# Optimization experiments

Measured on AMD Instinct MI355X. Metric: run time of the kernel, lower is better.

The kernel has to match this reference:

```python
import jax, jax.numpy as jnp
import numpy as np

N = 591   # number of drugs (hardcoded in the original module)
FD = 1024 # args.fd
E = 120000


def setup_inputs() -> dict:
    key = jax.random.key(0)
    ks = jax.random.split(key, 32)
    s = 1.0 / np.sqrt(FD).astype(np.float32)
    inp = {}
    inp['dm1'] = jax.random.normal(ks[0], (N, FD), jnp.float32)
    for i, v in enumerate(['t', 's', 'g']):
        inp['edges_' + v] = jax.random.randint(ks[1 + i], (2, E), 0, N)
        inp['ew_' + v] = jax.random.uniform(ks[4 + i], (E,), jnp.float32)
    for i, nm in enumerate(['t1', 't2', 's1', 's2', 'g1', 'g2']):
        inp['W_' + nm] = jax.random.normal(ks[7 + i], (FD, FD), jnp.float32) * s
        inp['b_' + nm] = jnp.zeros((FD,), jnp.float32)
    inp['fc1_w'] = jax.random.normal(ks[20], (30, 6), jnp.float32) * 0.4
    inp['fc1_b'] = jnp.zeros((30,), jnp.float32)
    inp['fc2_w'] = jax.random.normal(ks[21], (6, 30), jnp.float32) * 0.2
    inp['fc2_b'] = jnp.zeros((6,), jnp.float32)
    inp['conv_w'] = jax.random.normal(ks[22], (6,), jnp.float32) * 0.4
    inp['conv_b'] = jnp.zeros((), jnp.float32)
    return inp


def gcn(x, W, b, src, dst, ew):
    """PyG GCNConv: x@W, add self-loops (weight 1), symmetric norm, scatter-add, +bias."""
    xw = x @ W                                   # [N, FD]
    loop = jnp.arange(N)
    src2 = jnp.concatenate([src, loop])
    dst2 = jnp.concatenate([dst, loop])
    ew2 = jnp.concatenate([ew, jnp.ones((N,), ew.dtype)])
    deg = jax.ops.segment_sum(ew2, dst2, num_segments=N)
    dinv = jnp.where(deg > 0, jax.lax.rsqrt(deg), 0.0)
    norm = dinv[src2] * ew2 * dinv[dst2]         # [E+N]
    agg = jax.ops.segment_sum(norm[:, None] * xw[src2], dst2, num_segments=N)
    return agg + b


def reference(dm1, edges_t, ew_t, edges_s, ew_s, edges_g, ew_g,
              W_t1, b_t1, W_t2, b_t2, W_s1, b_s1, W_s2, b_s2,
              W_g1, b_g1, W_g2, b_g2,
              fc1_w, fc1_b, fc2_w, fc2_b, conv_w, conv_b):
    def two_layers(e, w, W1, b1, W2, b2):
        h1 = jax.nn.relu(gcn(dm1, W1, b1, e[0], e[1], w))
        h2 = jax.nn.relu(gcn(h1, W2, b2, e[0], e[1], w))
        return h1, h2

    t1, t2 = two_layers(edges_t, ew_t, W_t1, b_t1, W_t2, b_t2)
    s1, s2 = two_layers(edges_s, ew_s, W_s1, b_s1, W_s2, b_s2)
    g1, g2 = two_layers(edges_g, ew_g, W_g1, b_g1, W_g2, b_g2)

    # cat(dim=1).t().view(1, 6, FD, N)  ->  [6, FD, N]
    comb = jnp.stack([t1.T, t2.T, s1.T, s2.T, g1.T, g2.T], axis=0)

    # SE-style channel attention over the 6 channels
    pool = comb.mean(axis=(1, 2))                         # [6]
    h = jax.nn.relu(pool @ fc1_w.T + fc1_b)               # [30]
    a = jax.nn.sigmoid(h @ fc2_w.T + fc2_b)               # [6]
    att = jax.nn.relu(a[:, None, None] * comb)            # [6, FD, N]

    # 1x1 conv (6 -> 1 channel), then view(FD, N).t()
    y = jnp.einsum('c,cfn->fn', conv_w, att) + conv_b     # [FD, N]
    return y.T                                            # [N, FD]
```

## Files before the change

### kernel.cpp

```cpp
#include <hip/hip_runtime.h>

#define NDRUG 591
#define FDIM 1024
#define NEDGE 120000
#define MPAD 640
#define ASTRIDE 349281
#define ABSTRIDE (MPAD*MPAD)
#define HSTRIDE (MPAD*FDIM)
#define REAL (NDRUG*FDIM)
#define WSTRIDE (FDIM*FDIM)

typedef __attribute__((ext_vector_type(8))) short bf16x8;
typedef __attribute__((ext_vector_type(4))) float f32x4;
typedef __attribute__((ext_vector_type(4))) unsigned short u16x4;

static __device__ __forceinline__ unsigned short f2bf(float f) {
    unsigned u = __builtin_bit_cast(unsigned, f);
    u += 0x7fffu + ((u >> 16) & 1u);
    return (unsigned short)(u >> 16);
}
static __device__ __forceinline__ float bf2f(unsigned short h) {
    return __builtin_bit_cast(float, ((unsigned)h) << 16);
}

typedef const __attribute__((address_space(1))) unsigned int* gp1_t;
typedef __attribute__((address_space(3))) unsigned int* lp3_t;
static __device__ __forceinline__ void gload16(const void* g, unsigned short* l) {
    __builtin_amdgcn_global_load_lds((gp1_t)g, (lp3_t)l, 16, 0, 0);
}

__global__ void init_kernel(float* AmatF, float* scal) {
    int i = blockIdx.x * blockDim.x + threadIdx.x;
    const int TOT = 3 * ASTRIDE;
    int b = i * 4;
    if (b + 3 < TOT) {
        *(float4*)(AmatF + b) = make_float4(0.f, 0.f, 0.f, 0.f);
    } else if (b < TOT) {
        for (int j = b; j < TOT; ++j) AmatF[j] = 0.f;
    }
    if (i < 16) scal[i] = 0.f;
}

__global__ void scatter_kernel(const int* e_t, const float* w_t,
                               const int* e_s, const float* w_s,
                               const int* e_g, const float* w_g, float* AmatF) {
    int i = blockIdx.x * blockDim.x + threadIdx.x;
    const int PER = NEDGE + NDRUG;
    if (i >= 3 * PER) return;
    int g = i / PER, r = i - g * PER;
    float* Ag = AmatF + (long)g * ASTRIDE;
    if (r < NEDGE) {
        const int*   E_ = (g == 0) ? e_t : (g == 1) ? e_s : e_g;
        const float* W_ = (g == 0) ? w_t : (g == 1) ? w_s : w_g;
        int src = E_[r], dst = E_[NEDGE + r];
        atomicAdd(Ag + (long)dst * NDRUG + src, W_[r]);
    } else {
        int n = r - NEDGE;
        atomicAdd(Ag + (long)n * NDRUG + n, 1.0f);
    }
}

__global__ void rowdeg_kernel(const float* AmatF, float* dinv) {
    int r = blockIdx.x, g = blockIdx.y;
    const float* row = AmatF + (long)g * ASTRIDE + (long)r * NDRUG;
    float s = 0.f;
    for (int c = threadIdx.x; c < NDRUG; c += 64) s += row[c];
#pragma unroll
    for (int off = 32; off > 0; off >>= 1) s += __shfl_down(s, off);
    if (threadIdx.x == 0)
        dinv[g * NDRUG + r] = (s > 0.f) ? rsqrtf(s) : 0.f;
}

__global__ void conv_A(const float* AmatF, const float* dinv, unsigned short* Amatb) {
    int r = blockIdx.x, g = blockIdx.y;
    int t = threadIdx.x;
    if (t >= 160) return;
    int c = t * 4;
    u16x4 o = {0, 0, 0, 0};
    if (r < NDRUG) {
        const float* src = AmatF + (long)g * ASTRIDE + (long)r * NDRUG;
        const float* dv = dinv + g * NDRUG;
        float dr = dv[r];
#pragma unroll
        for (int j = 0; j < 4; j++) {
            int cc = c + j;
            if (cc < NDRUG) o[j] = f2bf(src[cc] * dv[cc] * dr);
        }
    }
    *(u16x4*)(Amatb + (long)g * ABSTRIDE + (long)r * MPAD + c) = o;
}

__global__ void conv_dm1(const float* dm1, unsigned short* dm1b) {
    int r = blockIdx.x;
    int c = threadIdx.x * 4;
    u16x4 o = {0, 0, 0, 0};
    if (r < NDRUG) {
        float4 v = *(const float4*)(dm1 + (long)r * FDIM + c);
        o[0] = f2bf(v.x); o[1] = f2bf(v.y); o[2] = f2bf(v.z); o[3] = f2bf(v.w);
    }
    *(u16x4*)(dm1b + (long)r * FDIM + c) = o;
}

__global__ void conv_w6(const float* w0, const float* w1, const float* w2,
                        const float* w3, const float* w4, const float* w5,
                        unsigned short* WTb) {
    __shared__ float s[32][33];
    int z = blockIdx.z;
    const float* W = (z == 0) ? w0 : (z == 1) ? w1 : (z == 2) ? w2
                   : (z == 3) ? w3 : (z == 4) ? w4 : w5;
    unsigned short* WT = WTb + (long)z * WSTRIDE;
    int n0 = blockIdx.x * 32, k0 = blockIdx.y * 32;
    int tx = threadIdx.x & 31, ty = threadIdx.x >> 5;
#pragma unroll
    for (int p = 0; p < 4; p++)
        s[ty + 8 * p][tx] = W[(long)(k0 + ty + 8 * p) * FDIM + n0 + tx];
    __syncthreads();
#pragma unroll
    for (int p = 0; p < 4; p++)
        WT[(long)(n0 + ty + 8 * p) * FDIM + k0 + tx] = f2bf(s[tx][ty + 8 * p]);
}

template <int EPI>
__global__ __launch_bounds__(256) void mfma_gemm(
    const unsigned short* __restrict__ Abase, long strideA, int ldaK,
    const unsigned short* __restrict__ Bbase, long strideB, int ldbK,
    const float* __restrict__ bias0, const float* __restrict__ bias1,
    const float* __restrict__ bias2,
    unsigned short* __restrict__ Cbase, long strideC, int ldC, int K,
    float* __restrict__ poolacc, int layer)
{
    __shared__ unsigned short ldsA[2][4096];
    __shared__ unsigned short ldsB[2][4096];
    __shared__ float red[4];

    const int g = blockIdx.z;
    const unsigned short* A = Abase + (long)g * strideA;
    const unsigned short* B = Bbase + (long)g * strideB;
    unsigned short* C = Cbase + (long)g * strideC;
    const float* bias = (g == 0) ? bias0 : (g == 1) ? bias1 : bias2;

    const int m0 = blockIdx.y * 64;
    const int n0 = blockIdx.x * 64;
    const int tid = threadIdx.x;
    const int w = tid >> 6, lane = tid & 63;
    const int l15 = lane & 15, lq = lane >> 4;
    const int wm = w >> 1, wn = w & 1;

    const int sr  = lane >> 3;
    const int kcs = 8 * ((lane & 7) ^ sr);
    const int segA0 = 2 * w, segA1 = 2 * w + 1;
    const int rA0 = segA0 * 8 + sr, rA1 = segA1 * 8 + sr;

    int offA[2][2], offB[2][2];
    {
        int ra0 = 32 * wm + l15, ra1 = ra0 + 16;
        int rb0 = 32 * wn + l15, rb1 = rb0 + 16;
        offA[0][0] = ra0 * 64 + ((lq    ) ^ (ra0 & 7)) * 8;
        offA[0][1] = ra0 * 64 + ((lq + 4) ^ (ra0 & 7)) * 8;
        offA[1][0] = ra1 * 64 + ((lq    ) ^ (ra1 & 7)) * 8;
        offA[1][1] = ra1 * 64 + ((lq + 4) ^ (ra1 & 7)) * 8;
        offB[0][0] = rb0 * 64 + ((lq    ) ^ (rb0 & 7)) * 8;
        offB[0][1] = rb0 * 64 + ((lq + 4) ^ (rb0 & 7)) * 8;
        offB[1][0] = rb1 * 64 + ((lq    ) ^ (rb1 & 7)) * 8;
        offB[1][1] = rb1 * 64 + ((lq + 4) ^ (rb1 & 7)) * 8;
    }

    f32x4 acc00 = {0.f, 0.f, 0.f, 0.f}, acc01 = {0.f, 0.f, 0.f, 0.f};
    f32x4 acc10 = {0.f, 0.f, 0.f, 0.f}, acc11 = {0.f, 0.f, 0.f, 0.f};

    const int nt = K >> 6;

#define STAGE(bf, k0c) do {                                                        \
    gload16(A + (long)(m0 + rA0) * ldaK + (k0c) + kcs, &ldsA[bf][segA0 * 512]);    \
    gload16(A + (long)(m0 + rA1) * ldaK + (k0c) + kcs, &ldsA[bf][segA1 * 512]);    \
    gload16(B + (long)(n0 + rA0) * ldbK + (k0c) + kcs, &ldsB[bf][segA0 * 512]);    \
    gload16(B + (long)(n0 + rA1) * ldbK + (k0c) + kcs, &ldsB[bf][segA1 * 512]);    \
} while (0)

    STAGE(0, 0);

    for (int t = 0; t < nt; ++t) {
        const int cur = t & 1;
        if (t + 1 < nt) {
            STAGE(cur ^ 1, (t + 1) << 6);
            asm volatile("s_waitcnt vmcnt(4)");
        } else {
            asm volatile("s_waitcnt vmcnt(0)");
        }
        __builtin_amdgcn_s_barrier();
        __builtin_amdgcn_sched_barrier(0);
        const unsigned short* pa = ldsA[cur];
        const unsigned short* pb = ldsB[cur];
        {
            bf16x8 a0 = *(const bf16x8*)(pa + offA[0][0]);
            bf16x8 a1 = *(const bf16x8*)(pa + offA[1][0]);
            bf16x8 b0 = *(const bf16x8*)(pb + offB[0][0]);
            bf16x8 b1 = *(const bf16x8*)(pb + offB[1][0]);
            acc00 = __builtin_amdgcn_mfma_f32_16x16x32_bf16(a0, b0, acc00, 0, 0, 0);
            acc01 = __builtin_amdgcn_mfma_f32_16x16x32_bf16(a0, b1, acc01, 0, 0, 0);
            acc10 = __builtin_amdgcn_mfma_f32_16x16x32_bf16(a1, b0, acc10, 0, 0, 0);
            acc11 = __builtin_amdgcn_mfma_f32_16x16x32_bf16(a1, b1, acc11, 0, 0, 0);
        }
        {
            bf16x8 a0 = *(const bf16x8*)(pa + offA[0][1]);
            bf16x8 a1 = *(const bf16x8*)(pa + offA[1][1]);
            bf16x8 b0 = *(const bf16x8*)(pb + offB[0][1]);
            bf16x8 b1 = *(const bf16x8*)(pb + offB[1][1]);
            acc00 = __builtin_amdgcn_mfma_f32_16x16x32_bf16(a0, b0, acc00, 0, 0, 0);
            acc01 = __builtin_amdgcn_mfma_f32_16x16x32_bf16(a0, b1, acc01, 0, 0, 0);
            acc10 = __builtin_amdgcn_mfma_f32_16x16x32_bf16(a1, b0, acc10, 0, 0, 0);
            acc11 = __builtin_amdgcn_mfma_f32_16x16x32_bf16(a1, b1, acc11, 0, 0, 0);
        }
        asm volatile("s_waitcnt lgkmcnt(0)");
        __builtin_amdgcn_sched_barrier(0);
        __builtin_amdgcn_s_barrier();
    }
#undef STAGE

    if (EPI == 0) {
#define TSTORE(accv, mo, no) do {                                   \
        int nn = n0 + 32 * wn + (no) * 16 + l15;                    \
        int mm = m0 + 32 * wm + (mo) * 16 + lq * 4;                 \
        u16x4 pk;                                                   \
        pk[0] = f2bf(accv[0]); pk[1] = f2bf(accv[1]);               \
        pk[2] = f2bf(accv[2]); pk[3] = f2bf(accv[3]);               \
        *(u16x4*)&C[(long)nn * ldC + mm] = pk;                      \
} while (0)
        TSTORE(acc00, 0, 0); TSTORE(acc01, 0, 1);
        TSTORE(acc10, 1, 0); TSTORE(acc11, 1, 1);
#undef TSTORE
    } else {
        float spool = 0.f;
#define NSTORE(accv, mo, no) do {                                   \
        int nn = n0 + 32 * wn + (no) * 16 + l15;                    \
        int mm = m0 + 32 * wm + (mo) * 16 + lq * 4;                 \
        float bs = bias[nn];                                        \
        _Pragma("unroll")                                           \
        for (int i = 0; i < 4; i++) {                               \
            float v = fmaxf(accv[i] + bs, 0.f);                     \
            C[(long)(mm + i) * ldC + nn] = f2bf(v);                 \
            if (mm + i < NDRUG) spool += v;                         \
        }                                                           \
} while (0)
        NSTORE(acc00, 0, 0); NSTORE(acc01, 0, 1);
        NSTORE(acc10, 1, 0); NSTORE(acc11, 1, 1);
#undef NSTORE
#pragma unroll
        for (int off = 32; off > 0; off >>= 1) spool += __shfl_down(spool, off);
        if (lane == 0) red[w] = spool;
        __syncthreads();
        if (tid == 0)
            atomicAdd(poolacc + 2 * g + layer, red[0] + red[1] + red[2] + red[3]);
    }
}

__global__ void mlp_kernel(const float* acc, const float* fc1w, const float* fc1b,
                           const float* fc2w, const float* fc2b, const float* convw,
                           float* wout) {
    __shared__ float hsh[30], plsh[6];
    int t = threadIdx.x;
    const float inv = 1.0f / (float)REAL;
    if (t < 6) plsh[t] = acc[t] * inv;
    __syncthreads();
    if (t < 30) {
        float s = fc1b[t];
#pragma unroll
        for (int c = 0; c < 6; c++) s += plsh[c] * fc1w[t * 6 + c];
        hsh[t] = fmaxf(s, 0.f);
    }
    __syncthreads();
    float hv = (t < 30) ? hsh[t] : 0.f;
    for (int j = 0; j < 6; j++) {
        float p = (t < 30) ? hv * fc2w[j * 30 + t] : 0.f;
#pragma unroll
        for (int off = 32; off > 0; off >>= 1) p += __shfl_down(p, off);
        if (t == 0) {
            float s = fc2b[j] + p;
            wout[j] = convw[j] / (1.f + expf(-s));
        }
    }
}

__global__ void combine_kernel(const unsigned short* h1b, const unsigned short* h2b,
                               const float* wv, const float* convb, float* out) {
    int i = blockIdx.x * 256 + threadIdx.x;
    const int nv = REAL / 8;
    if (i >= nv) return;
    float cb = convb[0];
    float r[8];
#pragma unroll
    for (int j = 0; j < 8; j++) r[j] = cb;
#define ACCCH(c, ptr) do {                                          \
        float wc = wv[c];                                           \
        bf16x8 v = *(const bf16x8*)((ptr) + (long)i * 8);           \
        _Pragma("unroll")                                           \
        for (int j = 0; j < 8; j++) r[j] += wc * bf2f((unsigned short)v[j]); \
} while (0)
    ACCCH(0, h1b);
    ACCCH(1, h2b);
    ACCCH(2, h1b + HSTRIDE);
    ACCCH(3, h2b + HSTRIDE);
    ACCCH(4, h1b + 2 * HSTRIDE);
    ACCCH(5, h2b + 2 * HSTRIDE);
#undef ACCCH
    float4 o0 = make_float4(r[0], r[1], r[2], r[3]);
    float4 o1 = make_float4(r[4], r[5], r[6], r[7]);
    *(float4*)(out + (long)i * 8) = o0;
    *(float4*)(out + (long)i * 8 + 4) = o1;
}

extern "C" void kernel_launch(void* const* d_in, const int* in_sizes, int n_in,
                              void* d_out, int out_size, void* d_ws, size_t ws_size,
                              hipStream_t stream) {
    const float* dm1 = (const float*)d_in[0];
    const int*   e_t = (const int*)d_in[1];
    const float* w_t = (const float*)d_in[2];
    const int*   e_s = (const int*)d_in[3];
    const float* w_s = (const float*)d_in[4];
    const int*   e_g = (const int*)d_in[5];
    const float* w_g = (const float*)d_in[6];
    const float* W_t1 = (const float*)d_in[7];
    const float* b_t1 = (const float*)d_in[8];
    const float* W_t2 = (const float*)d_in[9];
    const float* b_t2 = (const float*)d_in[10];
    const float* W_s1 = (const float*)d_in[11];
    const float* b_s1 = (const float*)d_in[12];
    const float* W_s2 = (const float*)d_in[13];
    const float* b_s2 = (const float*)d_in[14];
    const float* W_g1 = (const float*)d_in[15];
    const float* b_g1 = (const float*)d_in[16];
    const float* W_g2 = (const float*)d_in[17];
    const float* b_g2 = (const float*)d_in[18];
    const float* fc1w = (const float*)d_in[19];
    const float* fc1b = (const float*)d_in[20];
    const float* fc2w = (const float*)d_in[21];
    const float* fc2b = (const float*)d_in[22];
    const float* convw = (const float*)d_in[23];
    const float* convb = (const float*)d_in[24];
    float* out = (float*)d_out;

    char* base = (char*)d_ws;
    unsigned short* WTb = (unsigned short*)base;
    float* AmatF = (float*)base;
    unsigned short* h2b = (unsigned short*)(base + (size_t)3 * WSTRIDE * 2);
    size_t o = (size_t)6 * WSTRIDE * 2;
    float* dinv = (float*)(base + o); o += 8192;
    float* scal = (float*)(base + o); o += 256;
    unsigned short* dm1b  = (unsigned short*)(base + o); o += (size_t)MPAD * FDIM * 2;
    unsigned short* Amatb = (unsigned short*)(base + o); o += (size_t)3 * ABSTRIDE * 2;
    unsigned short* xwT   = (unsigned short*)(base + o); o += (size_t)3 * HSTRIDE * 2;
    unsigned short* h1b   = (unsigned short*)(base + o); o += (size_t)3 * HSTRIDE * 2;
    if (ws_size < o) return;

    init_kernel<<<(3 * ASTRIDE / 4 + 256) / 256, 256, 0, stream>>>(AmatF, scal);
    scatter_kernel<<<(3 * (NEDGE + NDRUG) + 255) / 256, 256, 0, stream>>>(
        e_t, w_t, e_s, w_s, e_g, w_g, AmatF);
    rowdeg_kernel<<<dim3(NDRUG, 3), 64, 0, stream>>>(AmatF, dinv);
    conv_A<<<dim3(MPAD, 3), 256, 0, stream>>>(AmatF, dinv, Amatb);
    conv_w6<<<dim3(32, 32, 6), 256, 0, stream>>>(
        W_t1, W_s1, W_g1, W_t2, W_s2, W_g2, WTb);
    conv_dm1<<<MPAD, 256, 0, stream>>>(dm1, dm1b);

    dim3 gg(FDIM / 64, MPAD / 64, 3);
    mfma_gemm<0><<<gg, 256, 0, stream>>>(
        dm1b, 0L, FDIM, WTb, (long)WSTRIDE, FDIM,
        nullptr, nullptr, nullptr, xwT, (long)HSTRIDE, MPAD, FDIM, scal, 0);
    mfma_gemm<1><<<gg, 256, 0, stream>>>(
        Amatb, (long)ABSTRIDE, MPAD, xwT, (long)HSTRIDE, MPAD,
        b_t1, b_s1, b_g1, h1b, (long)HSTRIDE, FDIM, MPAD, scal, 0);
    mfma_gemm<0><<<gg, 256, 0, stream>>>(
        h1b, (long)HSTRIDE, FDIM, WTb + (size_t)3 * WSTRIDE, (long)WSTRIDE, FDIM,
        nullptr, nullptr, nullptr, xwT, (long)HSTRIDE, MPAD, FDIM, scal, 0);
    mfma_gemm<1><<<gg, 256, 0, stream>>>(
        Amatb, (long)ABSTRIDE, MPAD, xwT, (long)HSTRIDE, MPAD,
        b_t2, b_s2, b_g2, h2b, (long)HSTRIDE, FDIM, MPAD, scal, 1);

    mlp_kernel<<<1, 64, 0, stream>>>(scal, fc1w, fc1b, fc2w, fc2b, convw, scal + 8);
    combine_kernel<<<(REAL / 8 + 255) / 256, 256, 0, stream>>>(h1b, h2b, scal + 8, convb, out);
}
```

Measured before the change: 219.0 us.

## Fuse all stages into one cooperative persistent kernel with grid syncs

Replaces the chain of about twelve kernel launches with a single cooperative kernel of 256 persistent blocks. The blocks step through the stages (zeroing, edge scatter, degree, bf16 conversions, the four GEMM phases, the MLP and the combine) separated by grid.sync, and the original launches remain as a fallback if the cooperative launch fails. This is meant to remove per-launch overhead and the idle gaps between launches. In exchange, parallelism is capped at 256 blocks; the GEMM phases have 480 tiles, so some blocks process two tiles. Each grid barrier also costs time, and the fused kernel may need more registers.

```diff
diff --git a/kernel.cpp b/kernel.cpp
--- a/kernel.cpp
+++ b/kernel.cpp
@@ -1,4 +1,6 @@
 #include <hip/hip_runtime.h>
+#include <hip/hip_cooperative_groups.h>
+namespace cg = cooperative_groups;
 
 #define NDRUG 591
 #define FDIM 1024
@@ -9,6 +11,10 @@
 #define HSTRIDE (MPAD*FDIM)
 #define REAL (NDRUG*FDIM)
 #define WSTRIDE (FDIM*FDIM)
+#define NBLK 256
+#define NTHR 256
+#define GSTR (NBLK*NTHR)
+#define NTILE 480
 
 typedef __attribute__((ext_vector_type(8))) short bf16x8;
 typedef __attribute__((ext_vector_type(4))) float f32x4;
@@ -29,118 +35,15 @@
     __builtin_amdgcn_global_load_lds((gp1_t)g, (lp3_t)l, 16, 0, 0);
 }
 
-__global__ void init_kernel(float* AmatF, float* scal) {
-    int i = blockIdx.x * blockDim.x + threadIdx.x;
-    const int TOT = 3 * ASTRIDE;
-    int b = i * 4;
-    if (b + 3 < TOT) {
-        *(float4*)(AmatF + b) = make_float4(0.f, 0.f, 0.f, 0.f);
-    } else if (b < TOT) {
-        for (int j = b; j < TOT; ++j) AmatF[j] = 0.f;
-    }
-    if (i < 16) scal[i] = 0.f;
-}
-
-__global__ void scatter_kernel(const int* e_t, const float* w_t,
-                               const int* e_s, const float* w_s,
-                               const int* e_g, const float* w_g, float* AmatF) {
-    int i = blockIdx.x * blockDim.x + threadIdx.x;
-    const int PER = NEDGE + NDRUG;
-    if (i >= 3 * PER) return;
-    int g = i / PER, r = i - g * PER;
-    float* Ag = AmatF + (long)g * ASTRIDE;
-    if (r < NEDGE) {
-        const int*   E_ = (g == 0) ? e_t : (g == 1) ? e_s : e_g;
-        const float* W_ = (g == 0) ? w_t : (g == 1) ? w_s : w_g;
-        int src = E_[r], dst = E_[NEDGE + r];
-        atomicAdd(Ag + (long)dst * NDRUG + src, W_[r]);
-    } else {
-        int n = r - NEDGE;
-        atomicAdd(Ag + (long)n * NDRUG + n, 1.0f);
-    }
-}
-
-__global__ void rowdeg_kernel(const float* AmatF, float* dinv) {
-    int r = blockIdx.x, g = blockIdx.y;
-    const float* row = AmatF + (long)g * ASTRIDE + (long)r * NDRUG;
-    float s = 0.f;
-    for (int c = threadIdx.x; c < NDRUG; c += 64) s += row[c];
-#pragma unroll
-    for (int off = 32; off > 0; off >>= 1) s += __shfl_down(s, off);
-    if (threadIdx.x == 0)
-        dinv[g * NDRUG + r] = (s > 0.f) ? rsqrtf(s) : 0.f;
-}
-
-__global__ void conv_A(const float* AmatF, const float* dinv, unsigned short* Amatb) {
-    int r = blockIdx.x, g = blockIdx.y;
-    int t = threadIdx.x;
-    if (t >= 160) return;
-    int c = t * 4;
-    u16x4 o = {0, 0, 0, 0};
-    if (r < NDRUG) {
-        const float* src = AmatF + (long)g * ASTRIDE + (long)r * NDRUG;
-        const float* dv = dinv + g * NDRUG;
-        float dr = dv[r];
-#pragma unroll
-        for (int j = 0; j < 4; j++) {
-            int cc = c + j;
-            if (cc < NDRUG) o[j] = f2bf(src[cc] * dv[cc] * dr);
-        }
-    }
-    *(u16x4*)(Amatb + (long)g * ABSTRIDE + (long)r * MPAD + c) = o;
-}
-
-__global__ void conv_dm1(const float* dm1, unsigned short* dm1b) {
-    int r = blockIdx.x;
-    int c = threadIdx.x * 4;
-    u16x4 o = {0, 0, 0, 0};
-    if (r < NDRUG) {
-        float4 v = *(const float4*)(dm1 + (long)r * FDIM + c);
-        o[0] = f2bf(v.x); o[1] = f2bf(v.y); o[2] = f2bf(v.z); o[3] = f2bf(v.w);
-    }
-    *(u16x4*)(dm1b + (long)r * FDIM + c) = o;
-}
-
-__global__ void conv_w6(const float* w0, const float* w1, const float* w2,
-                        const float* w3, const float* w4, const float* w5,
-                        unsigned short* WTb) {
-    __shared__ float s[32][33];
-    int z = blockIdx.z;
-    const float* W = (z == 0) ? w0 : (z == 1) ? w1 : (z == 2) ? w2
-                   : (z == 3) ? w3 : (z == 4) ? w4 : w5;
-    unsigned short* WT = WTb + (long)z * WSTRIDE;
-    int n0 = blockIdx.x * 32, k0 = blockIdx.y * 32;
-    int tx = threadIdx.x & 31, ty = threadIdx.x >> 5;
-#pragma unroll
-    for (int p = 0; p < 4; p++)
-        s[ty + 8 * p][tx] = W[(long)(k0 + ty + 8 * p) * FDIM + n0 + tx];
-    __syncthreads();
-#pragma unroll
-    for (int p = 0; p < 4; p++)
-        WT[(long)(n0 + ty + 8 * p) * FDIM + k0 + tx] = f2bf(s[tx][ty + 8 * p]);
-}
-
 template <int EPI>
-__global__ __launch_bounds__(256) void mfma_gemm(
-    const unsigned short* __restrict__ Abase, long strideA, int ldaK,
-    const unsigned short* __restrict__ Bbase, long strideB, int ldbK,
-    const float* __restrict__ bias0, const float* __restrict__ bias1,
-    const float* __restrict__ bias2,
-    unsigned short* __restrict__ Cbase, long strideC, int ldC, int K,
-    float* __restrict__ poolacc, int layer)
+static __device__ __forceinline__ void gemm_tile(
+    const unsigned short* __restrict__ A, int ldaK,
+    const unsigned short* __restrict__ B, int ldbK,
+    const float* __restrict__ bias,
+    unsigned short* __restrict__ C, int ldC, int K,
+    float* __restrict__ poolslot, int m0, int n0,
+    unsigned short (&ldsA)[2][4096], unsigned short (&ldsB)[2][4096], float* aux)
 {
-    __shared__ unsigned short ldsA[2][4096];
-    __shared__ unsigned short ldsB[2][4096];
-    __shared__ float red[4];
-
-    const int g = blockIdx.z;
-    const unsigned short* A = Abase + (long)g * strideA;
-    const unsigned short* B = Bbase + (long)g * strideB;
-    unsigned short* C = Cbase + (long)g * strideC;
-    const float* bias = (g == 0) ? bias0 : (g == 1) ? bias1 : bias2;
-
-    const int m0 = blockIdx.y * 64;
-    const int n0 = blockIdx.x * 64;
     const int tid = threadIdx.x;
     const int w = tid >> 6, lane = tid & 63;
     const int l15 = lane & 15, lq = lane >> 4;
@@ -165,9 +68,8 @@
         offB[1][1] = rb1 * 64 + ((lq + 4) ^ (rb1 & 7)) * 8;
     }
 
-    f32x4 acc00 = {0.f, 0.f, 0.f, 0.f}, acc01 = {0.f, 0.f, 0.f, 0.f};
-    f32x4 acc10 = {0.f, 0.f, 0.f, 0.f}, acc11 = {0.f, 0.f, 0.f, 0.f};
-
+    f32x4 acc00 = {0.f,0.f,0.f,0.f}, acc01 = {0.f,0.f,0.f,0.f};
+    f32x4 acc10 = {0.f,0.f,0.f,0.f}, acc11 = {0.f,0.f,0.f,0.f};
     const int nt = K >> 6;
 
 #define STAGE(bf, k0c) do {                                                        \
@@ -178,7 +80,6 @@
 } while (0)
 
     STAGE(0, 0);
-
     for (int t = 0; t < nt; ++t) {
         const int cur = t & 1;
         if (t + 1 < nt) {
@@ -247,11 +148,304 @@
 #undef NSTORE
 #pragma unroll
         for (int off = 32; off > 0; off >>= 1) spool += __shfl_down(spool, off);
-        if (lane == 0) red[w] = spool;
+        if (lane == 0) aux[w] = spool;
         __syncthreads();
-        if (tid == 0)
-            atomicAdd(poolacc + 2 * g + layer, red[0] + red[1] + red[2] + red[3]);
-    }
+        if (tid == 0) atomicAdd(poolslot, aux[0] + aux[1] + aux[2] + aux[3]);
+        __syncthreads();
+    }
+}
+
+struct MegaParams {
+    const float* dm1;
+    const int* et; const float* wt;
+    const int* es; const float* ws;
+    const int* eg; const float* wg;
+    const float* W[6];
+    const float* b1[3]; const float* b2[3];
+    const float* fc1w; const float* fc1b;
+    const float* fc2w; const float* fc2b;
+    const float* convw; const float* convb;
+    float* out;
+    float* AmatF; float* dinv; float* scal;
+    unsigned short* WTb; unsigned short* dm1b; unsigned short* Amatb;
+    unsigned short* xwT; unsigned short* h1b; unsigned short* h2b;
+};
+
+__global__ __launch_bounds__(256, 2) void mega(MegaParams p) {
+    __shared__ unsigned short ldsA[2][4096];
+    __shared__ unsigned short ldsB[2][4096];
+    __shared__ float aux[64];
+    cg::grid_group grid = cg::this_grid();
+    const int b = blockIdx.x, tid = threadIdx.x;
+
+    {
+        const int TOT = 3 * ASTRIDE;
+        for (int i = b * NTHR + tid; i * 4 < TOT; i += GSTR) {
+            int e = i * 4;
+            if (e + 3 < TOT) *(float4*)(p.AmatF + e) = make_float4(0.f, 0.f, 0.f, 0.f);
+            else { for (int j = e; j < TOT; ++j) p.AmatF[j] = 0.f; }
+        }
+        if (b == 0 && tid < 16) p.scal[tid] = 0.f;
+    }
+    grid.sync();
+
+    {
+        const int PER = NEDGE + NDRUG;
+        for (int i = b * NTHR + tid; i < 3 * PER; i += GSTR) {
+            int g = i / PER, r = i - g * PER;
+            float* Ag = p.AmatF + (long)g * ASTRIDE;
+            if (r < NEDGE) {
+                const int*   E_ = (g == 0) ? p.et : (g == 1) ? p.es : p.eg;
+                const float* W_ = (g == 0) ? p.wt : (g == 1) ? p.ws : p.wg;
+                atomicAdd(Ag + (long)E_[NEDGE + r] * NDRUG + E_[r], W_[r]);
+            } else {
+                int n = r - NEDGE;
+                atomicAdd(Ag + (long)n * NDRUG + n, 1.0f);
+            }
+        }
+    }
+    grid.sync();
+
+    {
+        int wv = tid >> 6, lane = tid & 63;
+        for (int row = b * 4 + wv; row < 3 * NDRUG; row += NBLK * 4) {
+            int g = row / NDRUG, r = row - g * NDRUG;
+            const float* src = p.AmatF + (long)g * ASTRIDE + (long)r * NDRUG;
+            float s = 0.f;
+            for (int c = lane; c < NDRUG; c += 64) s += src[c];
+#pragma unroll
+            for (int off = 32; off > 0; off >>= 1) s += __shfl_down(s, off);
+            if (lane == 0) p.dinv[row] = (s > 0.f) ? rsqrtf(s) : 0.f;
+        }
+    }
+    grid.sync();
+
+    {
+        for (int r = b; r < MPAD; r += NBLK) {
+            int c = tid * 4;
+            u16x4 o = {0, 0, 0, 0};
+            if (r < NDRUG) {
+                float4 v = *(const float4*)(p.dm1 + (long)r * FDIM + c);
+                o[0] = f2bf(v.x); o[1] = f2bf(v.y); o[2] = f2bf(v.z); o[3] = f2bf(v.w);
+            }
+            *(u16x4*)(p.dm1b + (long)r * FDIM + c) = o;
+        }
+        for (int it = b; it < 3 * MPAD; it += NBLK) {
+            int g = it / MPAD, r = it - g * MPAD;
+            if (tid < 160) {
+                int c = tid * 4;
+                u16x4 o = {0, 0, 0, 0};
+                if (r < NDRUG) {
+                    const float* src = p.AmatF + (long)g * ASTRIDE + (long)r * NDRUG;
+                    const float* dv = p.dinv + g * NDRUG;
+                    float dr = dv[r];
+#pragma unroll
+                    for (int j = 0; j < 4; j++) {
+                        int cc = c + j;
+                        if (cc < NDRUG) o[j] = f2bf(src[cc] * dv[cc] * dr);
+                    }
+                }
+                *(u16x4*)(p.Amatb + (long)g * ABSTRIDE + (long)r * MPAD + c) = o;
+            }
+        }
+        float* ts = (float*)ldsA;
+        int tx = tid & 31, ty = tid >> 5;
+        for (int tix = b; tix < 6 * 1024; tix += NBLK) {
+            int z = tix >> 10, rem = tix & 1023;
+            int n0w = (rem & 31) * 32, k0w = (rem >> 5) * 32;
+            const float* Wsrc = p.W[z];
+            unsigned short* WT = p.WTb + (long)z * WSTRIDE;
+            __syncthreads();
+#pragma unroll
+            for (int q = 0; q < 4; q++)
+                ts[(ty + 8 * q) * 33 + tx] = Wsrc[(long)(k0w + ty + 8 * q) * FDIM + n0w + tx];
+            __syncthreads();
+#pragma unroll
+            for (int q = 0; q < 4; q++)
+                WT[(long)(n0w + ty + 8 * q) * FDIM + k0w + tx] = f2bf(ts[tx * 33 + ty + 8 * q]);
+        }
+        __syncthreads();
+    }
+    grid.sync();
+
+#define TILE_LOOP(body) for (int tl = b; tl < NTILE; tl += NBLK) { \
+        int g = tl / 160, rr = tl - g * 160;                        \
+        int n0 = (rr & 15) * 64, m0 = (rr >> 4) * 64;               \
+        body;                                                       \
+    }
+
+    TILE_LOOP(gemm_tile<0>(p.dm1b, FDIM, p.WTb + (long)g * WSTRIDE, FDIM, nullptr,
+                           p.xwT + (long)g * HSTRIDE, MPAD, FDIM, nullptr, m0, n0, ldsA, ldsB, aux))
+    grid.sync();
+    TILE_LOOP(gemm_tile<1>(p.Amatb + (long)g * ABSTRIDE, MPAD, p.xwT + (long)g * HSTRIDE, MPAD,
+                           p.b1[g], p.h1b + (long)g * HSTRIDE, FDIM, MPAD,
+                           p.scal + 2 * g, m0, n0, ldsA, ldsB, aux))
+    grid.sync();
+    TILE_LOOP(gemm_tile<0>(p.h1b + (long)g * HSTRIDE, FDIM, p.WTb + (long)(3 + g) * WSTRIDE, FDIM,
+                           nullptr, p.xwT + (long)g * HSTRIDE, MPAD, FDIM, nullptr, m0, n0, ldsA, ldsB, aux))
+    grid.sync();
+    TILE_LOOP(gemm_tile<1>(p.Amatb + (long)g * ABSTRIDE, MPAD, p.xwT + (long)g * HSTRIDE, MPAD,
+                           p.b2[g], p.h2b + (long)g * HSTRIDE, FDIM, MPAD,
+                           p.scal + 2 * g + 1, m0, n0, ldsA, ldsB, aux))
+#undef TILE_LOOP
+    grid.sync();
+
+    if (b == 0) {
+        int t = tid;
+        const float inv = 1.0f / (float)REAL;
+        if (t < 6) aux[32 + t] = p.scal[t] * inv;
+        __syncthreads();
+        if (t < 30) {
+            float s = p.fc1b[t];
+#pragma unroll
+            for (int c = 0; c < 6; c++) s += aux[32 + c] * p.fc1w[t * 6 + c];
+            aux[t] = fmaxf(s, 0.f);
+        }
+        __syncthreads();
+        if (t < 64) {
+            float hv = (t < 30) ? aux[t] : 0.f;
+            for (int j = 0; j < 6; j++) {
+                float pr = (t < 30) ? hv * p.fc2w[j * 30 + t] : 0.f;
+#pragma unroll
+                for (int off = 32; off > 0; off >>= 1) pr += __shfl_down(pr, off);
+                if (t == 0)
+                    p.scal[8 + j] = p.convw[j] / (1.f + expf(-(p.fc2b[j] + pr)));
+            }
+        }
+    }
+    grid.sync();
+
+    {
+        const int nv = REAL / 8;
+        float cb = p.convb[0];
+        float w0 = p.scal[8], w1 = p.scal[9], w2 = p.scal[10];
+        float w3 = p.scal[11], w4 = p.scal[12], w5 = p.scal[13];
+        for (int i = b * NTHR + tid; i < nv; i += GSTR) {
+            float r8[8];
+#pragma unroll
+            for (int j = 0; j < 8; j++) r8[j] = cb;
+#define ACCCH(wc, ptr) do {                                                 \
+            bf16x8 v = *(const bf16x8*)((ptr) + (long)i * 8);               \
+            _Pragma("unroll")                                               \
+            for (int j = 0; j < 8; j++) r8[j] += (wc) * bf2f((unsigned short)v[j]); \
+} while (0)
+            ACCCH(w0, p.h1b);
+            ACCCH(w1, p.h2b);
+            ACCCH(w2, p.h1b + HSTRIDE);
+            ACCCH(w3, p.h2b + HSTRIDE);
+            ACCCH(w4, p.h1b + 2 * HSTRIDE);
+            ACCCH(w5, p.h2b + 2 * HSTRIDE);
+#undef ACCCH
+            *(float4*)(p.out + (long)i * 8)     = make_float4(r8[0], r8[1], r8[2], r8[3]);
+            *(float4*)(p.out + (long)i * 8 + 4) = make_float4(r8[4], r8[5], r8[6], r8[7]);
+        }
+    }
+}
+
+__global__ void init_kernel(float* AmatF, float* scal) {
+    int i = blockIdx.x * blockDim.x + threadIdx.x;
+    const int TOT = 3 * ASTRIDE;
+    int b = i * 4;
+    if (b + 3 < TOT) *(float4*)(AmatF + b) = make_float4(0.f, 0.f, 0.f, 0.f);
+    else if (b < TOT) { for (int j = b; j < TOT; ++j) AmatF[j] = 0.f; }
+    if (i < 16) scal[i] = 0.f;
+}
+
+__global__ void scatter_kernel(const int* e_t, const float* w_t,
+                               const int* e_s, const float* w_s,
+                               const int* e_g, const float* w_g, float* AmatF) {
+    int i = blockIdx.x * blockDim.x + threadIdx.x;
+    const int PER = NEDGE + NDRUG;
+    if (i >= 3 * PER) return;
+    int g = i / PER, r = i - g * PER;
+    float* Ag = AmatF + (long)g * ASTRIDE;
+    if (r < NEDGE) {
+        const int*   E_ = (g == 0) ? e_t : (g == 1) ? e_s : e_g;
+        const float* W_ = (g == 0) ? w_t : (g == 1) ? w_s : w_g;
+        atomicAdd(Ag + (long)E_[NEDGE + r] * NDRUG + E_[r], W_[r]);
+    } else {
+        int n = r - NEDGE;
+        atomicAdd(Ag + (long)n * NDRUG + n, 1.0f);
+    }
+}
+
+__global__ void rowdeg_kernel(const float* AmatF, float* dinv) {
+    int r = blockIdx.x, g = blockIdx.y;
+    const float* row = AmatF + (long)g * ASTRIDE + (long)r * NDRUG;
+    float s = 0.f;
+    for (int c = threadIdx.x; c < NDRUG; c += 64) s += row[c];
+#pragma unroll
+    for (int off = 32; off > 0; off >>= 1) s += __shfl_down(s, off);
+    if (threadIdx.x == 0) dinv[g * NDRUG + r] = (s > 0.f) ? rsqrtf(s) : 0.f;
+}
+
+__global__ void conv_A(const float* AmatF, const float* dinv, unsigned short* Amatb) {
+    int r = blockIdx.x, g = blockIdx.y;
+    int t = threadIdx.x;
+    if (t >= 160) return;
+    int c = t * 4;
+    u16x4 o = {0, 0, 0, 0};
+    if (r < NDRUG) {
+        const float* src = AmatF + (long)g * ASTRIDE + (long)r * NDRUG;
+        const float* dv = dinv + g * NDRUG;
+        float dr = dv[r];
+#pragma unroll
+        for (int j = 0; j < 4; j++) {
+            int cc = c + j;
+            if (cc < NDRUG) o[j] = f2bf(src[cc] * dv[cc] * dr);
+        }
+    }
+    *(u16x4*)(Amatb + (long)g * ABSTRIDE + (long)r * MPAD + c) = o;
+}
+
+__global__ void conv_dm1(const float* dm1, unsigned short* dm1b) {
+    int r = blockIdx.x;
+    int c = threadIdx.x * 4;
+    u16x4 o = {0, 0, 0, 0};
+    if (r < NDRUG) {
+        float4 v = *(const float4*)(dm1 + (long)r * FDIM + c);
+        o[0] = f2bf(v.x); o[1] = f2bf(v.y); o[2] = f2bf(v.z); o[3] = f2bf(v.w);
+    }
+    *(u16x4*)(dm1b + (long)r * FDIM + c) = o;
+}
+
+__global__ void conv_w6(const float* w0, const float* w1, const float* w2,
+                        const float* w3, const float* w4, const float* w5,
+                        unsigned short* WTb) {
+    __shared__ float s[32][33];
+    int z = blockIdx.z;
+    const float* W = (z == 0) ? w0 : (z == 1) ? w1 : (z == 2) ? w2
+                   : (z == 3) ? w3 : (z == 4) ? w4 : w5;
+    unsigned short* WT = WTb + (long)z * WSTRIDE;
+    int n0 = blockIdx.x * 32, k0 = blockIdx.y * 32;
+    int tx = threadIdx.x & 31, ty = threadIdx.x >> 5;
+#pragma unroll
+    for (int q = 0; q < 4; q++)
+        s[ty + 8 * q][tx] = W[(long)(k0 + ty + 8 * q) * FDIM + n0 + tx];
+    __syncthreads();
+#pragma unroll
+    for (int q = 0; q < 4; q++)
+        WT[(long)(n0 + ty + 8 * q) * FDIM + k0 + tx] = f2bf(s[tx][ty + 8 * q]);
+}
+
+template <int EPI>
+__global__ __launch_bounds__(256) void gemm_wrap(
+    const unsigned short* __restrict__ Abase, long strideA, int ldaK,
+    const unsigned short* __restrict__ Bbase, long strideB, int ldbK,
+    const float* __restrict__ bias0, const float* __restrict__ bias1,
+    const float* __restrict__ bias2,
+    unsigned short* __restrict__ Cbase, long strideC, int ldC, int K,
+    float* __restrict__ poolacc, int layer)
+{
+    __shared__ unsigned short ldsA[2][4096];
+    __shared__ unsigned short ldsB[2][4096];
+    __shared__ float aux[64];
+    int g = blockIdx.z;
+    const float* bias = (g == 0) ? bias0 : (g == 1) ? bias1 : bias2;
+    gemm_tile<EPI>(Abase + (long)g * strideA, ldaK, Bbase + (long)g * strideB, ldbK, bias,
+                   Cbase + (long)g * strideC, ldC, K,
+                   poolacc ? poolacc + 2 * g + layer : nullptr,
+                   blockIdx.y * 64, blockIdx.x * 64, ldsA, ldsB, aux);
 }
 
 __global__ void mlp_kernel(const float* acc, const float* fc1w, const float* fc1b,
@@ -271,13 +465,10 @@
     __syncthreads();
     float hv = (t < 30) ? hsh[t] : 0.f;
     for (int j = 0; j < 6; j++) {
-        float p = (t < 30) ? hv * fc2w[j * 30 + t] : 0.f;
-#pragma unroll
-        for (int off = 32; off > 0; off >>= 1) p += __shfl_down(p, off);
-        if (t == 0) {
-            float s = fc2b[j] + p;
-            wout[j] = convw[j] / (1.f + expf(-s));
-        }
+        float pr = (t < 30) ? hv * fc2w[j * 30 + t] : 0.f;
+#pragma unroll
+        for (int off = 32; off > 0; off >>= 1) pr += __shfl_down(pr, off);
+        if (t == 0) wout[j] = convw[j] / (1.f + expf(-(fc2b[j] + pr)));
     }
 }
 
@@ -287,14 +478,14 @@
     const int nv = REAL / 8;
     if (i >= nv) return;
     float cb = convb[0];
-    float r[8];
-#pragma unroll
-    for (int j = 0; j < 8; j++) r[j] = cb;
+    float r8[8];
+#pragma unroll
+    for (int j = 0; j < 8; j++) r8[j] = cb;
 #define ACCCH(c, ptr) do {                                          \
         float wc = wv[c];                                           \
         bf16x8 v = *(const bf16x8*)((ptr) + (long)i * 8);           \
         _Pragma("unroll")                                           \
-        for (int j = 0; j < 8; j++) r[j] += wc * bf2f((unsigned short)v[j]); \
+        for (int j = 0; j < 8; j++) r8[j] += wc * bf2f((unsigned short)v[j]); \
 } while (0)
     ACCCH(0, h1b);
     ACCCH(1, h2b);
@@ -303,78 +494,73 @@
     ACCCH(4, h1b + 2 * HSTRIDE);
     ACCCH(5, h2b + 2 * HSTRIDE);
 #undef ACCCH
-    float4 o0 = make_float4(r[0], r[1], r[2], r[3]);
-    float4 o1 = make_float4(r[4], r[5], r[6], r[7]);
-    *(float4*)(out + (long)i * 8) = o0;
-    *(float4*)(out + (long)i * 8 + 4) = o1;
+    *(float4*)(out + (long)i * 8)     = make_float4(r8[0], r8[1], r8[2], r8[3]);
+    *(float4*)(out + (long)i * 8 + 4) = make_float4(r8[4], r8[5], r8[6], r8[7]);
 }
 
 extern "C" void kernel_launch(void* const* d_in, const int* in_sizes, int n_in,
                               void* d_out, int out_size, void* d_ws, size_t ws_size,
                               hipStream_t stream) {
-    const float* dm1 = (const float*)d_in[0];
-    const int*   e_t = (const int*)d_in[1];
-    const float* w_t = (const float*)d_in[2];
-    const int*   e_s = (const int*)d_in[3];
-    const float* w_s = (const float*)d_in[4];
-    const int*   e_g = (const int*)d_in[5];
-    const float* w_g = (const float*)d_in[6];
-    const float* W_t1 = (const float*)d_in[7];
-    const float* b_t1 = (const float*)d_in[8];
-    const float* W_t2 = (const float*)d_in[9];
-    const float* b_t2 = (const float*)d_in[10];
-    const float* W_s1 = (const float*)d_in[11];
-    const float* b_s1 = (const float*)d_in[12];
-    const float* W_s2 = (const float*)d_in[13];
-    const float* b_s2 = (const float*)d_in[14];
-    const float* W_g1 = (const float*)d_in[15];
-    const float* b_g1 = (const float*)d_in[16];
-    const float* W_g2 = (const float*)d_in[17];
-    const float* b_g2 = (const float*)d_in[18];
-    const float* fc1w = (const float*)d_in[19];
-    const float* fc1b = (const float*)d_in[20];
-    const float* fc2w = (const float*)d_in[21];
-    const float* fc2b = (const float*)d_in[22];
-    const float* convw = (const float*)d_in[23];
-    const float* convb = (const float*)d_in[24];
-    float* out = (float*)d_out;
+    MegaParams p;
+    p.dm1 = (const float*)d_in[0];
+    p.et = (const int*)d_in[1];  p.wt = (const float*)d_in[2];
+    p.es = (const int*)d_in[3];  p.ws = (const float*)d_in[4];
+    p.eg = (const int*)d_in[5];  p.wg = (const float*)d_in[6];
+    p.W[0] = (const float*)d_in[7];   p.b1[0] = (const float*)d_in[8];
+    p.W[3] = (const float*)d_in[9];   p.b2[0] = (const float*)d_in[10];
+    p.W[1] = (const float*)d_in[11];  p.b1[1] = (const float*)d_in[12];
+    p.W[4] = (const float*)d_in[13];  p.b2[1] = (const float*)d_in[14];
+    p.W[2] = (const float*)d_in[15];  p.b1[2] = (const float*)d_in[16];
+    p.W[5] = (const float*)d_in[17];  p.b2[2] = (const float*)d_in[18];
+    p.fc1w = (const float*)d_in[19]; p.fc1b = (const float*)d_in[20];
+    p.fc2w = (const float*)d_in[21]; p.fc2b = (const float*)d_in[22];
+    p.convw = (const float*)d_in[23]; p.convb = (const float*)d_in[24];
+    p.out = (float*)d_out;
 
     char* base = (char*)d_ws;
-    unsigned short* WTb = (unsigned short*)base;
-    float* AmatF = (float*)base;
-    unsigned short* h2b = (unsigned short*)(base + (size_t)3 * WSTRIDE * 2);
-    size_t o = (size_t)6 * WSTRIDE * 2;
-    float* dinv = (float*)(base + o); o += 8192;
-    float* scal = (float*)(base + o); o += 256;
-    unsigned short* dm1b  = (unsigned short*)(base + o); o += (size_t)MPAD * FDIM * 2;
-    unsigned short* Amatb = (unsigned short*)(base + o); o += (size_t)3 * ABSTRIDE * 2;
-    unsigned short* xwT   = (unsigned short*)(base + o); o += (size_t)3 * HSTRIDE * 2;
-    unsigned short* h1b   = (unsigned short*)(base + o); o += (size_t)3 * HSTRIDE * 2;
+    size_t o = 0;
+    auto alloc = [&](size_t bytes) { void* ptr = base + o; o += (bytes + 255) & ~(size_t)255; return ptr; };
+    p.AmatF = (float*)alloc((size_t)3 * ASTRIDE * 4);
+    p.WTb   = (unsigned short*)alloc((size_t)6 * WSTRIDE * 2);
+    p.dinv  = (float*)alloc(8192);
+    p.scal  = (float*)alloc(256);
+    p.dm1b  = (unsigned short*)alloc((size_t)MPAD * FDIM * 2);
+    p.Amatb = (unsigned short*)alloc((size_t)3 * ABSTRIDE * 2);
+    p.xwT   = (unsigned short*)alloc((size_t)3 * HSTRIDE * 2);
+    p.h1b   = (unsigned short*)alloc((size_t)3 * HSTRIDE * 2);
+    p.h2b   = (unsigned short*)alloc((size_t)3 * HSTRIDE * 2);
     if (ws_size < o) return;
 
-    init_kernel<<<(3 * ASTRIDE / 4 + 256) / 256, 256, 0, stream>>>(AmatF, scal);
+    void* args[] = { (void*)&p };
+    hipError_t err = hipLaunchCooperativeKernel((const void*)mega, dim3(NBLK), dim3(NTHR),
+                                                args, 0, stream);
+    if (err == hipSuccess) return;
+
+    init_kernel<<<(3 * ASTRIDE / 4 + 256) / 256, 256, 0, stream>>>(p.AmatF, p.scal);
     scatter_kernel<<<(3 * (NEDGE + NDRUG) + 255) / 256, 256, 0, stream>>>(
-        e_t, w_t, e_s, w_s, e_g, w_g, AmatF);
-    rowdeg_kernel<<<dim3(NDRUG, 3), 64, 0, stream>>>(AmatF, dinv);
-    conv_A<<<dim3(MPAD, 3), 256, 0, stream>>>(AmatF, dinv, Amatb);
+        p.et, p.wt, p.es, p.ws, p.eg, p.wg, p.AmatF);
+    rowdeg_kernel<<<dim3(NDRUG, 3), 64, 0, stream>>>(p.AmatF, p.dinv);
+    conv_A<<<dim3(MPAD, 3), 256, 0, stream>>>(p.AmatF, p.dinv, p.Amatb);
     conv_w6<<<dim3(32, 32, 6), 256, 0, stream>>>(
-        W_t1, W_s1, W_g1, W_t2, W_s2, W_g2, WTb);
-    conv_dm1<<<MPAD, 256, 0, stream>>>(dm1, dm1b);
+        p.W[0], p.W[1], p.W[2], p.W[3], p.W[4], p.W[5], p.WTb);
+    conv_dm1<<<MPAD, 256, 0, stream>>>(p.dm1, p.dm1b);
 
     dim3 gg(FDIM / 64, MPAD / 64, 3);
-    mfma_gemm<0><<<gg, 256, 0, stream>>>(
-        dm1b, 0L, FDIM, WTb, (long)WSTRIDE, FDIM,
-        nullptr, nullptr, nullptr, xwT, (long)HSTRIDE, MPAD, FDIM, scal, 0);
-    mfma_gemm<1><<<gg, 256, 0, stream>>>(
-        Amatb, (long)ABSTRIDE, MPAD, xwT, (long)HSTRIDE, MPAD,
-        b_t1, b_s1, b_g1, h1b, (long)HSTRIDE, FDIM, MPAD, scal, 0);
-    mfma_gemm<0><<<gg, 256, 0, stream>>>(
-        h1b, (long)HSTRIDE, FDIM, WTb + (size_t)3 * WSTRIDE, (long)WSTRIDE, FDIM,
-        nullptr, nullptr, nullptr, xwT, (long)HSTRIDE, MPAD, FDIM, scal, 0);
-    mfma_gemm<1><<<gg, 256, 0, stream>>>(
-        Amatb, (long)ABSTRIDE, MPAD, xwT, (long)HSTRIDE, MPAD,
-        b_t2, b_s2, b_g2, h2b, (long)HSTRIDE, FDIM, MPAD, scal, 1);
-
-    mlp_kernel<<<1, 64, 0, stream>>>(scal, fc1w, fc1b, fc2w, fc2b, convw, scal + 8);
-    combine_kernel<<<(REAL / 8 + 255) / 256, 256, 0, stream>>>(h1b, h2b, scal + 8, convb, out);
-}
+    gemm_wrap<0><<<gg, 256, 0, stream>>>(
+        p.dm1b, 0L, FDIM, p.WTb, (long)WSTRIDE, FDIM,
+        nullptr, nullptr, nullptr, p.xwT, (long)HSTRIDE, MPAD, FDIM, p.scal, 0);
+    gemm_wrap<1><<<gg, 256, 0, stream>>>(
+        p.Amatb, (long)ABSTRIDE, MPAD, p.xwT, (long)HSTRIDE, MPAD,
+        p.b1[0], p.b1[1], p.b1[2], p.h1b, (long)HSTRIDE, FDIM, MPAD, p.scal, 0);
+    gemm_wrap<0><<<gg, 256, 0, stream>>>(
+        p.h1b, (long)HSTRIDE, FDIM, p.WTb + (size_t)3 * WSTRIDE, (long)WSTRIDE, FDIM,
+        nullptr, nullptr, nullptr, p.xwT, (long)HSTRIDE, MPAD, FDIM, p.scal, 0);
+    gemm_wrap<1><<<gg, 256, 0, stream>>>(
+        p.Amatb, (long)ABSTRIDE, MPAD, p.xwT, (long)HSTRIDE, MPAD,
+        p.b2[0], p.b2[1], p.b2[2], p.h2b, (long)HSTRIDE, FDIM, MPAD, p.scal, 1);
+
+    mlp_kernel<<<1, 64, 0, stream>>>(p.scal, p.fc1w, p.fc1b, p.fc2w, p.fc2b, p.convw,
+                                     p.scal + 8);
+    combine_kernel<<<(REAL / 8 + 255) / 256, 256, 0, stream>>>(p.h1b, p.h2b, p.scal + 8,
+                                                               p.convb, p.out);
+}
```

Measured after the change: 521.0 us. +137.9%, slower.
